# Optimization experiments

Measured on AMD Instinct MI355X. Metric: run time of the kernel, lower is better.

The kernel has to match this reference:

```python
import jax, jax.numpy as jnp
import numpy as np

SEQ, VOCAB, HID, OUT = 8192, 256, 2048, 256


def setup_inputs() -> dict:
    key = jax.random.key(0)
    ks = jax.random.split(key, 21)
    def lin(kw, fan_in, shape):
        return (jax.random.normal(kw, shape, dtype=jnp.float32) / np.sqrt(fan_in)).astype(jnp.float32)
    inp = {
        "x": jax.random.randint(ks[0], (SEQ, 1), 0, VOCAB, dtype=jnp.int64 if jax.config.read("jax_enable_x64") else jnp.int32),
        "emb": jax.random.normal(ks[1], (VOCAB, VOCAB), dtype=jnp.float32),
        "W_i": lin(ks[2], VOCAB, (VOCAB, HID)), "b_i": lin(ks[3], VOCAB, (HID,)),
        "U_i": lin(ks[4], HID, (HID, HID)),   "c_i": lin(ks[5], HID, (HID,)),
        "W_f": lin(ks[6], VOCAB, (VOCAB, HID)), "b_f": lin(ks[7], VOCAB, (HID,)),
        "U_f": lin(ks[8], HID, (HID, HID)),   "c_f": lin(ks[9], HID, (HID,)),
        "W_g": lin(ks[10], VOCAB, (VOCAB, HID)), "b_g": lin(ks[11], VOCAB, (HID,)),
        "U_g": lin(ks[12], HID, (HID, HID)),  "c_g": lin(ks[13], HID, (HID,)),
        "W_o": lin(ks[14], VOCAB, (VOCAB, HID)), "b_o": lin(ks[15], VOCAB, (HID,)),
        "U_o": lin(ks[16], HID, (HID, HID)),  "c_o": lin(ks[17], HID, (HID,)),
        "V_w": lin(ks[18], HID, (HID, OUT)),  "V_b": lin(ks[19], HID, (OUT,)),
    }
    return inp


def reference(x, emb, W_i, b_i, U_i, c_i, W_f, b_f, U_f, c_f,
              W_g, b_g, U_g, c_g, W_o, b_o, U_o, c_o, V_w, V_b):
    H = U_i.shape[0]
    # embedding lookup: (S,1) ids -> (S,1,V)
    x_emb = emb[x[:, 0]][:, None, :]
    # precompute all input projections (the W_* matmuls are time-independent)
    gi = x_emb @ W_i + b_i  # (S,1,H)
    gf = x_emb @ W_f + b_f
    gg = x_emb @ W_g + b_g
    go = x_emb @ W_o + b_o

    def step(carry, gates):
        h, c = carry  # (1,H) each
        zi, zf, zg, zo = gates
        i = jax.nn.sigmoid(zi + h @ U_i + c_i)
        f = jax.nn.sigmoid(zf + h @ U_f + c_f)
        g = jnp.tanh(zg + h @ U_g + c_g)
        o = jax.nn.sigmoid(zo + h @ U_o + c_o)
        c_new = f * c + i * g
        h_new = o * jnp.tanh(c_new)
        return (h_new, c_new), h_new

    h0 = jnp.zeros((1, H), dtype=x_emb.dtype)
    c0 = jnp.zeros((1, H), dtype=x_emb.dtype)
    (h_T, c_T), hs = jax.lax.scan(step, (h0, c0), (gi, gf, gg, go))
    out = hs @ V_w + V_b  # (S,1,OUT)
    return out, (jax.lax.stop_gradient(h_T), jax.lax.stop_gradient(c_T))
```

## Files before the change

### kernel.cpp

```cpp
#include <hip/hip_runtime.h>

#define SEQ   8192
#define VOCAB 256
#define HID   2048
#define ODIM  256
#define NBLK  256
#define NTHR  512
#define JPB   8

typedef unsigned int v4u __attribute__((ext_vector_type(4)));

__device__ __forceinline__ void ld32_2q(const void* pE, const void* pO,
                                        v4u& r0, v4u& r1) {
    asm volatile("global_load_dwordx4 %0, %2, off sc1\n\t"
                 "global_load_dwordx4 %1, %3, off sc1\n\t"
                 "s_waitcnt vmcnt(0)"
                 : "=&v"(r0), "=&v"(r1) : "v"(pE), "v"(pO) : "memory");
}

__device__ __forceinline__ void atomic_swap_pub(unsigned long long* p,
                                                unsigned long long v) {
    asm volatile("global_atomic_swap_x2 %0, %1, off sc1"
                 :: "v"(p), "v"(v) : "memory");
}

__device__ __forceinline__ float fsigmoid(float x) {
    return __builtin_amdgcn_rcpf(1.f + __expf(-x));
}
__device__ __forceinline__ float ftanh(float x) {
    x = fminf(20.f, fmaxf(-20.f, x));
    float e = __expf(2.f * x);
    return (e - 1.f) * __builtin_amdgcn_rcpf(e + 1.f);
}

__device__ __forceinline__ float dpp_ror4(float v) {
    return __int_as_float(__builtin_amdgcn_update_dpp(
        0, __float_as_int(v), 0x124, 0xF, 0xF, false));
}
__device__ __forceinline__ float dpp_ror8(float v) {
    return __int_as_float(__builtin_amdgcn_update_dpp(
        0, __float_as_int(v), 0x128, 0xF, 0xF, false));
}

__global__ void k_zv(const float* __restrict__ emb, const float* __restrict__ W,
                     const float* __restrict__ bb, const float* __restrict__ cb,
                     float* __restrict__ Zv, int gate) {
    __shared__ float e[32][VOCAB];
    const int tid = threadIdx.x;
    const int vt = blockIdx.x, ct = blockIdx.y;
    for (int r = 0; r < 32; ++r)
        e[r][tid] = emb[(size_t)(vt * 32 + r) * VOCAB + tid];
    __syncthreads();
    const int j = ct * 256 + tid;
    const float bias = bb[j] + cb[j];
    float acc[32];
#pragma unroll
    for (int r = 0; r < 32; ++r) acc[r] = 0.f;
    for (int u = 0; u < VOCAB; ++u) {
        float w = W[(size_t)u * HID + j];
#pragma unroll
        for (int r = 0; r < 32; ++r) acc[r] += e[r][u] * w;
    }
    for (int r = 0; r < 32; ++r)
        Zv[(size_t)(vt * 32 + r) * (4 * HID) + (size_t)gate * HID + j] = acc[r] + bias;
}

__launch_bounds__(NTHR, 2)
__global__ void k_lstm(const float* __restrict__ Uii, const float* __restrict__ Uff,
                       const float* __restrict__ Ugg, const float* __restrict__ Uoo,
                       const float* __restrict__ Zv,  const int* __restrict__ x,
                       unsigned long long* pub, float* __restrict__ hs,
                       float* __restrict__ outTail) {
    __shared__ __align__(16) float hpad[128 * 20];
    __shared__ __align__(16) float scr2[2][32 * 36];

    const int tid  = threadIdx.x;
    const int b    = blockIdx.x;
    const int gate = tid & 3;
    const int rs   = tid >> 2;
    const int lane = tid & 63;
    const int wv   = tid >> 6;
    const int jg   = b * JPB + wv;

    const float* Ug = (gate == 0) ? Uii : (gate == 1) ? Uff : (gate == 2) ? Ugg : Uoo;

    float u[16][JPB];
#pragma unroll
    for (int r = 0; r < 16; ++r) {
        const float4* p = (const float4*)(Ug + (size_t)(rs * 16 + r) * HID + b * JPB);
        float4 a0 = p[0], a1 = p[1];
        u[r][0] = a0.x; u[r][1] = a0.y; u[r][2] = a0.z; u[r][3] = a0.w;
        u[r][4] = a1.x; u[r][5] = a1.y; u[r][6] = a1.z; u[r][7] = a1.w;
    }

    const size_t pslot = (size_t)((wv & 2) ? 1024 : 0) + 4 * b + 2 * ((wv >> 2) & 1) + (wv & 1);

    float4* hp4 = (float4*)hpad;
    float creg = 0.f;
    unsigned budget = 1u << 22;

    for (int t = 0; t < SEQ; ++t) {
        const int xt = x[t];
        float zx = Zv[(size_t)xt * (4 * HID) + (size_t)gate * HID + jg];

        float4 hv;
        if (t == 0) {
            hv = make_float4(0.f, 0.f, 0.f, 0.f);
        } else {
            const unsigned tgt = (unsigned)t;
            const unsigned long long* slE = pub + (size_t)(t & 1) * 2048 + tid * 2;
            const unsigned long long* slO = slE + 1024;
            v4u Q0, Q1;
            ld32_2q(slE, slO, Q0, Q1);
            while (!((Q0.y == tgt) & (Q0.w == tgt) &
                     (Q1.y == tgt) & (Q1.w == tgt)) && budget != 0) {
                --budget;
                __builtin_amdgcn_s_sleep(1);
                ld32_2q(slE, slO, Q0, Q1);
            }
            hv.x = __uint_as_float(Q0.x);
            hv.y = __uint_as_float(Q0.z);
            hv.z = __uint_as_float(Q1.x);
            hv.w = __uint_as_float(Q1.z);
        }

        *(float4*)&hpad[(tid >> 2) * 20 + (tid & 3) * 4] = hv;
        __threadfence_block();

        float acc[JPB];
#pragma unroll
        for (int jj = 0; jj < JPB; ++jj) acc[jj] = 0.f;
#pragma unroll
        for (int k = 0; k < 4; ++k) {
            float4 h4 = hp4[rs * 5 + k];
            float hvv[4] = {h4.x, h4.y, h4.z, h4.w};
#pragma unroll
            for (int i = 0; i < 4; ++i)
#pragma unroll
                for (int jj = 0; jj < JPB; ++jj)
                    acc[jj] += hvv[i] * u[k * 4 + i][jj];
        }

#pragma unroll
        for (int jj = 0; jj < JPB; ++jj) {
            acc[jj] += dpp_ror4(acc[jj]);
            acc[jj] += dpp_ror8(acc[jj]);
        }
        if ((lane & 12) == 0) {
            const int chunk = wv * 4 + (lane >> 4);
            float* p = &scr2[t & 1][chunk * 36 + gate * JPB];
            *(float4*)(p)     = make_float4(acc[0], acc[1], acc[2], acc[3]);
            *(float4*)(p + 4) = make_float4(acc[4], acc[5], acc[6], acc[7]);
        }
        __syncthreads();

        {
            const int c = lane >> 2;
            const float* s = &scr2[t & 1][0];
            float z = s[c * 36 + gate * JPB + wv] +
                      s[(c + 16) * 36 + gate * JPB + wv];
            z += dpp_ror4(z);
            z += dpp_ror8(z);
            z += __shfl_xor(z, 16);
            z += __shfl_xor(z, 32);
            z += zx;
            float zi = __shfl(z, 0);
            float zf = __shfl(z, 1);
            float zg = __shfl(z, 2);
            float zo = __shfl(z, 3);
            float ig = fsigmoid(zi);
            float fg = fsigmoid(zf);
            float gg = ftanh(zg);
            float og = fsigmoid(zo);
            float cn = fg * creg + ig * gg;
            float hn = og * ftanh(cn);
            creg = cn;
            if (lane == 0) {
                unsigned long long pk =
                    ((unsigned long long)(unsigned)(t + 1) << 32) | __float_as_uint(hn);
                atomic_swap_pub(&pub[(size_t)((t + 1) & 1) * 2048 + pslot], pk);
                hs[(size_t)t * HID + jg] = hn;
                if (t == SEQ - 1) { outTail[jg] = hn; outTail[HID + jg] = cn; }
            }
        }
    }
}

__global__ void k_out(const float* __restrict__ hs, const float* __restrict__ Vw,
                      const float* __restrict__ Vb, float* __restrict__ out) {
    __shared__ float tile[32][64];
    const int tid = threadIdx.x;
    const int t0 = blockIdx.x * 32;
    float acc[32];
#pragma unroll
    for (int r = 0; r < 32; ++r) acc[r] = 0.f;
    for (int k0 = 0; k0 < HID; k0 += 64) {
        {
            const int r = tid >> 3, kk = (tid & 7) * 8;
            const float4* p = (const float4*)(hs + (size_t)(t0 + r) * HID + k0 + kk);
            float4 a = p[0], bq = p[1];
            *(float4*)&tile[r][kk]     = a;
            *(float4*)&tile[r][kk + 4] = bq;
        }
        __syncthreads();
        for (int kk = 0; kk < 64; ++kk) {
            float w = Vw[(size_t)(k0 + kk) * ODIM + tid];
#pragma unroll
            for (int r = 0; r < 32; ++r) acc[r] += tile[r][kk] * w;
        }
        __syncthreads();
    }
    const float vb = Vb[tid];
    for (int r = 0; r < 32; ++r)
        out[(size_t)(t0 + r) * ODIM + tid] = acc[r] + vb;
}

extern "C" void kernel_launch(void* const* d_in, const int* in_sizes, int n_in,
                              void* d_out, int out_size, void* d_ws, size_t ws_size,
                              hipStream_t stream) {
    const int*   x   = (const int*)d_in[0];
    const float* emb = (const float*)d_in[1];
    const float* W[4] = {(const float*)d_in[2], (const float*)d_in[6],
                         (const float*)d_in[10], (const float*)d_in[14]};
    const float* B[4] = {(const float*)d_in[3], (const float*)d_in[7],
                         (const float*)d_in[11], (const float*)d_in[15]};
    const float* U[4] = {(const float*)d_in[4], (const float*)d_in[8],
                         (const float*)d_in[12], (const float*)d_in[16]};
    const float* C[4] = {(const float*)d_in[5], (const float*)d_in[9],
                         (const float*)d_in[13], (const float*)d_in[17]};
    const float* Vw = (const float*)d_in[18];
    const float* Vb = (const float*)d_in[19];
    float* out = (float*)d_out;

    float* ws = (float*)d_ws;
    float* Zv = ws;
    float* hs = Zv + (size_t)VOCAB * 4 * HID;
    unsigned long long* pub = (unsigned long long*)(hs + (size_t)SEQ * HID);

    for (int g = 0; g < 4; ++g)
        k_zv<<<dim3(8, 8), dim3(256), 0, stream>>>(emb, W[g], B[g], C[g], Zv, g);

    float* outTail = out + (size_t)SEQ * ODIM;
    const float *Ui = U[0], *Uf = U[1], *Ugp = U[2], *Uo = U[3];
    const float* Zvc = Zv; const int* xc = x;
    unsigned long long* pubc = pub; float* hsc = hs; float* ot = outTail;
    void* args[9] = {&Ui, &Uf, &Ugp, &Uo, &Zvc, &xc, &pubc, &hsc, &ot};
    (void)hipLaunchCooperativeKernel((void*)k_lstm, dim3(NBLK), dim3(NTHR), args, 0, stream);

    k_out<<<dim3(256), dim3(256), 0, stream>>>(hs, Vw, Vb, out);
}
```

Before: 15.76 ms.

## Use contiguous publish layout and sentinel-slot polling for hidden state exchange

Changes the per-step publication of h from a permuted slot layout to a contiguous one indexed by hidden column, so each thread reads its four values with one base address and an offset. Waiting threads now poll a single pseudo-randomly chosen 8-byte sentinel slot instead of repeatedly reloading the full 32 bytes, and reload the full chunk only once that sentinel is fresh. The next token id is also prefetched a step ahead. This aims to cut polling traffic and latency on the grid-wide per-timestep sync, but adds a possible extra reload round trip when the sentinel flips before the thread's own slots do.

New measurement: 43.00 ms. 2.73x slower.

```diff
diff --git a/kernel.cpp b/kernel.cpp
--- a/kernel.cpp
+++ b/kernel.cpp
@@ -9,13 +9,29 @@
 #define JPB   8
 
 typedef unsigned int v4u __attribute__((ext_vector_type(4)));
-
-__device__ __forceinline__ void ld32_2q(const void* pE, const void* pO,
-                                        v4u& r0, v4u& r1) {
+typedef unsigned int v2u __attribute__((ext_vector_type(2)));
+
+__device__ __forceinline__ void ld_probe0(const void* pl, const void* sp,
+                                          v4u& q0, v4u& q1, v2u& s) {
+    asm volatile("global_load_dwordx4 %0, %3, off sc1\n\t"
+                 "global_load_dwordx4 %1, %3, off offset:16 sc1\n\t"
+                 "global_load_dwordx2 %2, %4, off sc1\n\t"
+                 "s_waitcnt vmcnt(0)"
+                 : "=&v"(q0), "=&v"(q1), "=&v"(s)
+                 : "v"(pl), "v"(sp) : "memory");
+}
+
+__device__ __forceinline__ void ld8_coh(const void* p, v2u& r) {
+    asm volatile("global_load_dwordx2 %0, %1, off sc1\n\t"
+                 "s_waitcnt vmcnt(0)"
+                 : "=&v"(r) : "v"(p) : "memory");
+}
+
+__device__ __forceinline__ void ld32_coh(const void* p, v4u& r0, v4u& r1) {
     asm volatile("global_load_dwordx4 %0, %2, off sc1\n\t"
-                 "global_load_dwordx4 %1, %3, off sc1\n\t"
+                 "global_load_dwordx4 %1, %2, off offset:16 sc1\n\t"
                  "s_waitcnt vmcnt(0)"
-                 : "=&v"(r0), "=&v"(r1) : "v"(pE), "v"(pO) : "memory");
+                 : "=&v"(r0), "=&v"(r1) : "v"(p) : "memory");
 }
 
 __device__ __forceinline__ void atomic_swap_pub(unsigned long long* p,
@@ -93,30 +109,41 @@
         u[r][4] = a1.x; u[r][5] = a1.y; u[r][6] = a1.z; u[r][7] = a1.w;
     }
 
-    const size_t pslot = (size_t)((wv & 2) ? 1024 : 0) + 4 * b + 2 * ((wv >> 2) & 1) + (wv & 1);
-
     float4* hp4 = (float4*)hpad;
     float creg = 0.f;
     unsigned budget = 1u << 22;
+    int xt = x[0];
 
     for (int t = 0; t < SEQ; ++t) {
-        const int xt = x[t];
         float zx = Zv[(size_t)xt * (4 * HID) + (size_t)gate * HID + jg];
+        int xt_n = (t + 1 < SEQ) ? x[t + 1] : 0;
 
         float4 hv;
         if (t == 0) {
             hv = make_float4(0.f, 0.f, 0.f, 0.f);
         } else {
             const unsigned tgt = (unsigned)t;
-            const unsigned long long* slE = pub + (size_t)(t & 1) * 2048 + tid * 2;
-            const unsigned long long* slO = slE + 1024;
-            v4u Q0, Q1;
-            ld32_2q(slE, slO, Q0, Q1);
-            while (!((Q0.y == tgt) & (Q0.w == tgt) &
-                     (Q1.y == tgt) & (Q1.w == tgt)) && budget != 0) {
-                --budget;
-                __builtin_amdgcn_s_sleep(1);
-                ld32_2q(slE, slO, Q0, Q1);
+            const unsigned long long* pl = pub + (size_t)(t & 1) * HID + 4 * tid;
+            const int scol = (int)(((unsigned)(b + 37 * t)) & 255u) * JPB + wv;
+            const unsigned long long* sp = pub + (size_t)(t & 1) * HID + scol;
+            v4u Q0, Q1; v2u S;
+            ld_probe0(pl, sp, Q0, Q1, S);
+            bool fresh = (Q0.y == tgt) & (Q0.w == tgt) &
+                         (Q1.y == tgt) & (Q1.w == tgt);
+            if (!fresh) {
+                while (S.y != tgt && budget != 0) {
+                    --budget;
+                    __builtin_amdgcn_s_sleep(1);
+                    ld8_coh(sp, S);
+                }
+                for (;;) {
+                    ld32_coh(pl, Q0, Q1);
+                    fresh = (Q0.y == tgt) & (Q0.w == tgt) &
+                            (Q1.y == tgt) & (Q1.w == tgt);
+                    if (fresh || budget == 0) break;
+                    --budget;
+                    __builtin_amdgcn_s_sleep(1);
+                }
             }
             hv.x = __uint_as_float(Q0.x);
             hv.y = __uint_as_float(Q0.z);
@@ -178,11 +205,12 @@
             if (lane == 0) {
                 unsigned long long pk =
                     ((unsigned long long)(unsigned)(t + 1) << 32) | __float_as_uint(hn);
-                atomic_swap_pub(&pub[(size_t)((t + 1) & 1) * 2048 + pslot], pk);
+                atomic_swap_pub(&pub[(size_t)((t + 1) & 1) * HID + jg], pk);
                 hs[(size_t)t * HID + jg] = hn;
                 if (t == SEQ - 1) { outTail[jg] = hn; outTail[HID + jg] = cn; }
             }
         }
+        xt = xt_n;
     }
 }
 
```
